# Performance work log

Hardware: AMD Instinct MI355X
Metric: run time of the kernel (lower is better)

## Reference

```python
import math
import jax, jax.numpy as jnp
import numpy as np


def setup_inputs() -> dict:
    key = jax.random.key(0)
    kq, kk, kv = jax.random.split(key, 3)
    bs, n_tok, n_heads, width = 2, 2048, 8, 64
    deg = 32  # neighbors per dst token -> coo_cnt_max
    q = jax.random.normal(kq, (bs, n_tok, n_heads, width), dtype=jnp.float32)
    k = jax.random.normal(kk, (bs, n_tok, n_heads, width), dtype=jnp.float32)
    v = jax.random.normal(kv, (bs, n_tok, n_heads, width), dtype=jnp.float32)
    rng = np.random.default_rng(0)
    dst = np.repeat(np.arange(n_tok), deg)            # [cl]
    src = rng.integers(0, n_tok, size=n_tok * deg)    # [cl]
    sm = np.tile(np.arange(deg), n_tok)               # [cl], unique per dst
    coo = jnp.asarray(np.stack([dst, src, sm], axis=1), dtype=jnp.int32)  # [cl,3]
    return {"q": q, "k": k, "v": v, "coo": coo, "coo_cnt_max": deg}


def reference(q, k, v, coo, coo_cnt_max):
    bs, n_tok, n_heads, width = q.shape
    dst, src, sm = coo[:, 0], coo[:, 1], coo[:, 2]
    # [b, h, t, w] layout
    qq = q.transpose(0, 2, 1, 3)
    kk = k.transpose(0, 2, 1, 3)
    vv = v.transpose(0, 2, 1, 3)
    scale = -1.0 / math.sqrt(width)
    # per-edge negative scaled L1 distance: [b, h, cl]
    ww = jnp.sum(jnp.abs(qq[:, :, dst, :] - kk[:, :, src, :]), axis=-1) * scale
    neg_big = jnp.asarray(-1e32, dtype=q.dtype)
    # scatter edge scores into dense padded attention slots: [b, h, t, cnt+1]
    attn = jnp.full((bs, n_heads, n_tok, coo_cnt_max + 1), neg_big, dtype=q.dtype)
    attn = attn.at[:, :, dst, sm].set(ww)
    attn_sm = jax.nn.softmax(attn, axis=-1)
    # scatter values into padded neighbor-value tensor: [b, h, t, cnt+1, w]
    vw = jnp.zeros((bs, n_heads, n_tok, coo_cnt_max + 1, width), dtype=q.dtype)
    vw = vw.at[:, :, dst, sm, :].set(vv[:, :, src, :])
    vo = jnp.einsum('bhds,bhdsw->bdhw', attn_sm, vw)
    # only dst tokens appearing in coo receive output; others stay zero
    vout = jnp.zeros_like(v).at[:, dst, :, :].set(vo[:, dst, :, :])
    return vout
```

## Files before the change

kernel.cpp:

```cpp
#include <hip/hip_runtime.h>

#define BS   2
#define NT   2048
#define NH   8
#define WD   64
#define DEG  32

__global__ __launch_bounds__(64) void l1attn_sparse_kernel(
    const float* __restrict__ q,
    const float* __restrict__ k,
    const float* __restrict__ v,
    const int* __restrict__ coo,
    float* __restrict__ out)
{
    const int bid   = blockIdx.x;
    const int combo = bid & 7;
    const int hp    = combo & 3;
    const int b     = combo >> 2;
    const int t     = bid >> 3;
    const int ln    = threadIdx.x;
    const int hw    = ln >> 5;
    const int l     = ln & 31;

    __shared__ int   s_src[DEG];
    __shared__ float s_q[2 * WD];
    __shared__ float s_k[DEG * 2 * WD];

    if (ln < DEG) {
        s_src[ln] = coo[(t * DEG + ln) * 3 + 1];
    }
    {
        const float2* qrow = (const float2*)
            (q + ((size_t)(b * NT + t) * NH + hp * 2) * WD);
        float2 qv = qrow[ln];
        s_q[2 * ln]     = qv.x;
        s_q[2 * ln + 1] = qv.y;
    }
    __syncthreads();

    {
        const int c = l;
        #pragma unroll
        for (int r = 0; r < 16; ++r) {
            const int j = 2 * r + hw;
            const int s = s_src[j];
            const int chunk = (c + j) & 31;
            const float* gaddr = k + ((size_t)(b * NT + s) * NH + hp * 2) * WD
                               + chunk * 4;
            float* laddr = s_k + 2 * r * (2 * WD);
            __builtin_amdgcn_global_load_lds(
                (const __attribute__((address_space(1))) void*)gaddr,
                (__attribute__((address_space(3))) void*)laddr,
                16, 0, 0);
        }
    }

    const int h  = hp * 2 + hw;
    const int jg = l >> 4;
    const int wq = l & 15;
    float4 vr[16];
    #pragma unroll
    for (int i = 0; i < 16; ++i) {
        const int sv = s_src[2 * i + jg];
        vr[i] = *(const float4*)(v + ((size_t)(b * NT + sv) * NH + h) * WD + 4 * wq);
    }

    __syncthreads();

    const float* qh = s_q + hw * WD;
    float acc = 0.f;
    #pragma unroll
    for (int i = 0; i < 16; ++i) {
        const int slot = ((hw * 16 + i) - l) & 31;
        float4 kv = *(const float4*)(s_k + l * (2 * WD) + slot * 4);
        const int wb = i * 4;
        acc += fabsf(qh[wb]     - kv.x);
        acc += fabsf(qh[wb + 1] - kv.y);
        acc += fabsf(qh[wb + 2] - kv.z);
        acc += fabsf(qh[wb + 3] - kv.w);
    }
    float logit = -0.125f * acc;

    float m = logit;
    #pragma unroll
    for (int d = 16; d >= 1; d >>= 1) m = fmaxf(m, __shfl_xor(m, d));
    float e = __expf(logit - m);
    float ssum = e;
    #pragma unroll
    for (int d = 16; d >= 1; d >>= 1) ssum += __shfl_xor(ssum, d);
    const float p = e / ssum;

    float4 o4 = make_float4(0.f, 0.f, 0.f, 0.f);
    #pragma unroll
    for (int i = 0; i < 16; ++i) {
        const float pj = __shfl(p, 2 * i + jg, 32);
        o4.x += pj * vr[i].x;
        o4.y += pj * vr[i].y;
        o4.z += pj * vr[i].z;
        o4.w += pj * vr[i].w;
    }
    o4.x += __shfl_xor(o4.x, 16);
    o4.y += __shfl_xor(o4.y, 16);
    o4.z += __shfl_xor(o4.z, 16);
    o4.w += __shfl_xor(o4.w, 16);

    if (jg == 0) {
        *(float4*)(out + ((size_t)(b * NT + t) * NH + h) * WD + 4 * wq) = o4;
    }
}

extern "C" void kernel_launch(void* const* d_in, const int* in_sizes, int n_in,
                              void* d_out, int out_size, void* d_ws, size_t ws_size,
                              hipStream_t stream) {
    const float* q   = (const float*)d_in[0];
    const float* k   = (const float*)d_in[1];
    const float* v   = (const float*)d_in[2];
    const int*   coo = (const int*)d_in[3];
    float*       o   = (float*)d_out;

    dim3 grid(BS * NT * 4);
    dim3 block(64);
    hipLaunchKernelGGL(l1attn_sparse_kernel, grid, block, 0, stream, q, k, v, coo, o);
}
```

Baseline: 106.3 us.

## Pre-pack K and V to bf16 interleaved rows and gather both via LDS

Adds a pre-pass kernel that converts K and V to bf16 and packs them into one 512-byte row per (batch, head-pair, token) in workspace. The main kernel then gathers a single packed row per neighbor into LDS, covering both K and V, and reads V from LDS instead of doing separate per-thread global loads. This halves gather traffic for the random neighbor accesses. It costs an extra kernel launch plus a full pass over K and V, and bf16 rounding reduces accuracy. The fp32 path is kept as a fallback when the workspace is too small.

```diff
diff --git a/kernel.cpp b/kernel.cpp
--- a/kernel.cpp
+++ b/kernel.cpp
@@ -1,4 +1,5 @@
 #include <hip/hip_runtime.h>
+#include <hip/hip_bf16.h>
 
 #define BS   2
 #define NT   2048
@@ -6,7 +7,136 @@
 #define WD   64
 #define DEG  32
 
-__global__ __launch_bounds__(64) void l1attn_sparse_kernel(
+#define PK_ROWS   (BS * 4 * NT)
+#define PK_ROW_B  512
+#define PK_UINTS  (PK_ROWS * (PK_ROW_B / 4))
+
+__device__ __forceinline__ float bfbits_lo(unsigned int u) {
+    unsigned int x = u << 16; float f; __builtin_memcpy(&f, &x, 4); return f;
+}
+__device__ __forceinline__ float bfbits_hi(unsigned int u) {
+    unsigned int x = u & 0xffff0000u; float f; __builtin_memcpy(&f, &x, 4); return f;
+}
+__device__ __forceinline__ unsigned short f2bf(float f) {
+    __hip_bfloat16 h = __float2bfloat16(f);
+    unsigned short u; __builtin_memcpy(&u, &h, 2); return u;
+}
+
+__global__ __launch_bounds__(256) void pack_kv_bf16(
+    const float* __restrict__ k,
+    const float* __restrict__ v,
+    unsigned int* __restrict__ packed)
+{
+    const int u    = blockIdx.x * 256 + threadIdx.x;
+    const int row  = u >> 7;
+    const int pos  = u & 127;
+    const int part = pos >> 6;
+    const int e    = pos & 63;
+    const int s    = row & (NT - 1);
+    const int hp   = (row >> 11) & 3;
+    const int b    = row >> 13;
+    const int elem = e * 2;
+    const int h_in = elem >> 6;
+    const int w0   = elem & 63;
+
+    const float* src = (part == 0 ? k : v)
+        + (((size_t)(b * NT + s) * NH + hp * 2 + h_in) << 6) + w0;
+    float2 f = *(const float2*)src;
+    packed[u] = (unsigned int)f2bf(f.x) | ((unsigned int)f2bf(f.y) << 16);
+}
+
+__global__ __launch_bounds__(64) void l1attn_main_bf16(
+    const float* __restrict__ q,
+    const unsigned int* __restrict__ packed,
+    const int* __restrict__ coo,
+    float* __restrict__ out)
+{
+    const int bid   = blockIdx.x;
+    const int combo = bid & 7;
+    const int hp    = combo & 3;
+    const int b     = combo >> 2;
+    const int t     = bid >> 3;
+    const int ln    = threadIdx.x;
+    const int hw    = ln >> 5;
+    const int l     = ln & 31;
+
+    __shared__ int          s_src[DEG];
+    __shared__ float        s_q[2 * WD];
+    __shared__ unsigned int s_k[DEG * 128];
+
+    if (ln < DEG) {
+        s_src[ln] = coo[(t * DEG + ln) * 3 + 1];
+    }
+    {
+        const float2* qrow = (const float2*)
+            (q + ((size_t)(b * NT + t) * NH + hp * 2) * WD);
+        float2 qv = qrow[ln];
+        s_q[2 * ln]     = qv.x;
+        s_q[2 * ln + 1] = qv.y;
+    }
+    __syncthreads();
+
+    {
+        #pragma unroll
+        for (int r = 0; r < 16; ++r) {
+            const int j = 2 * r + hw;
+            const int s = s_src[j];
+            const int chunk = (l + j) & 31;
+            const char* gaddr = (const char*)packed
+                + ((size_t)((b * 4 + hp) * NT + s)) * PK_ROW_B + chunk * 16;
+            char* laddr = (char*)s_k + 2 * r * PK_ROW_B;
+            __builtin_amdgcn_global_load_lds(
+                (const __attribute__((address_space(1))) void*)gaddr,
+                (__attribute__((address_space(3))) void*)laddr,
+                16, 0, 0);
+        }
+    }
+    __syncthreads();
+
+    const float* qh = s_q + hw * WD;
+    float acc = 0.f;
+    #pragma unroll
+    for (int i = 0; i < 8; ++i) {
+        const int slot = ((hw * 8 + i) - l) & 31;
+        uint4 c = *(const uint4*)((const char*)s_k + l * PK_ROW_B + slot * 16);
+        const int wb = i * 8;
+        const unsigned int ws[4] = {c.x, c.y, c.z, c.w};
+        #pragma unroll
+        for (int m = 0; m < 4; ++m) {
+            acc += fabsf(qh[wb + 2 * m]     - bfbits_lo(ws[m]));
+            acc += fabsf(qh[wb + 2 * m + 1] - bfbits_hi(ws[m]));
+        }
+    }
+    float logit = -0.125f * acc;
+
+    float m = logit;
+    #pragma unroll
+    for (int d = 16; d >= 1; d >>= 1) m = fmaxf(m, __shfl_xor(m, d));
+    float e = __expf(logit - m);
+    float ssum = e;
+    #pragma unroll
+    for (int d = 16; d >= 1; d >>= 1) ssum += __shfl_xor(ssum, d);
+    const float p = e / ssum;
+
+    const int gv   = 16 + hw * 8 + (l >> 2);
+    const int boff = (l & 3) * 4;
+    float o0 = 0.f, o1 = 0.f;
+    #pragma unroll 8
+    for (int j = 0; j < DEG; ++j) {
+        const float pj = __shfl(p, j, 32);
+        const int slot = (gv - j) & 31;
+        unsigned int w = *(const unsigned int*)
+            ((const char*)s_k + j * PK_ROW_B + slot * 16 + boff);
+        o0 += pj * bfbits_lo(w);
+        o1 += pj * bfbits_hi(w);
+    }
+
+    const int h = hp * 2 + hw;
+    float2 res = make_float2(o0, o1);
+    *(float2*)(out + ((size_t)(b * NT + t) * NH + h) * WD + 2 * l) = res;
+}
+
+__global__ __launch_bounds__(64) void l1attn_sparse_fp32(
     const float* __restrict__ q,
     const float* __restrict__ k,
     const float* __restrict__ v,
@@ -26,18 +156,14 @@
     __shared__ float s_q[2 * WD];
     __shared__ float s_k[DEG * 2 * WD];
 
-    if (ln < DEG) {
-        s_src[ln] = coo[(t * DEG + ln) * 3 + 1];
-    }
+    if (ln < DEG) s_src[ln] = coo[(t * DEG + ln) * 3 + 1];
     {
         const float2* qrow = (const float2*)
             (q + ((size_t)(b * NT + t) * NH + hp * 2) * WD);
         float2 qv = qrow[ln];
-        s_q[2 * ln]     = qv.x;
-        s_q[2 * ln + 1] = qv.y;
-    }
-    __syncthreads();
-
+        s_q[2 * ln] = qv.x; s_q[2 * ln + 1] = qv.y;
+    }
+    __syncthreads();
     {
         const int c = l;
         #pragma unroll
@@ -50,11 +176,9 @@
             float* laddr = s_k + 2 * r * (2 * WD);
             __builtin_amdgcn_global_load_lds(
                 (const __attribute__((address_space(1))) void*)gaddr,
-                (__attribute__((address_space(3))) void*)laddr,
-                16, 0, 0);
+                (__attribute__((address_space(3))) void*)laddr, 16, 0, 0);
         }
     }
-
     const int h  = hp * 2 + hw;
     const int jg = l >> 4;
     const int wq = l & 15;
@@ -64,9 +188,7 @@
         const int sv = s_src[2 * i + jg];
         vr[i] = *(const float4*)(v + ((size_t)(b * NT + sv) * NH + h) * WD + 4 * wq);
     }
-
-    __syncthreads();
-
+    __syncthreads();
     const float* qh = s_q + hw * WD;
     float acc = 0.f;
     #pragma unroll
@@ -74,13 +196,10 @@
         const int slot = ((hw * 16 + i) - l) & 31;
         float4 kv = *(const float4*)(s_k + l * (2 * WD) + slot * 4);
         const int wb = i * 4;
-        acc += fabsf(qh[wb]     - kv.x);
-        acc += fabsf(qh[wb + 1] - kv.y);
-        acc += fabsf(qh[wb + 2] - kv.z);
-        acc += fabsf(qh[wb + 3] - kv.w);
+        acc += fabsf(qh[wb] - kv.x) + fabsf(qh[wb + 1] - kv.y)
+             + fabsf(qh[wb + 2] - kv.z) + fabsf(qh[wb + 3] - kv.w);
     }
     float logit = -0.125f * acc;
-
     float m = logit;
     #pragma unroll
     for (int d = 16; d >= 1; d >>= 1) m = fmaxf(m, __shfl_xor(m, d));
@@ -89,24 +208,17 @@
     #pragma unroll
     for (int d = 16; d >= 1; d >>= 1) ssum += __shfl_xor(ssum, d);
     const float p = e / ssum;
-
     float4 o4 = make_float4(0.f, 0.f, 0.f, 0.f);
     #pragma unroll
     for (int i = 0; i < 16; ++i) {
         const float pj = __shfl(p, 2 * i + jg, 32);
-        o4.x += pj * vr[i].x;
-        o4.y += pj * vr[i].y;
-        o4.z += pj * vr[i].z;
-        o4.w += pj * vr[i].w;
-    }
-    o4.x += __shfl_xor(o4.x, 16);
-    o4.y += __shfl_xor(o4.y, 16);
-    o4.z += __shfl_xor(o4.z, 16);
-    o4.w += __shfl_xor(o4.w, 16);
-
-    if (jg == 0) {
+        o4.x += pj * vr[i].x; o4.y += pj * vr[i].y;
+        o4.z += pj * vr[i].z; o4.w += pj * vr[i].w;
+    }
+    o4.x += __shfl_xor(o4.x, 16); o4.y += __shfl_xor(o4.y, 16);
+    o4.z += __shfl_xor(o4.z, 16); o4.w += __shfl_xor(o4.w, 16);
+    if (jg == 0)
         *(float4*)(out + ((size_t)(b * NT + t) * NH + h) * WD + 4 * wq) = o4;
-    }
 }
 
 extern "C" void kernel_launch(void* const* d_in, const int* in_sizes, int n_in,
@@ -118,7 +230,14 @@
     const int*   coo = (const int*)d_in[3];
     float*       o   = (float*)d_out;
 
-    dim3 grid(BS * NT * 4);
-    dim3 block(64);
-    hipLaunchKernelGGL(l1attn_sparse_kernel, grid, block, 0, stream, q, k, v, coo, o);
-}
+    if (ws_size >= (size_t)PK_UINTS * 4) {
+        unsigned int* packed = (unsigned int*)d_ws;
+        hipLaunchKernelGGL(pack_kv_bf16, dim3(PK_UINTS / 256), dim3(256), 0,
+                           stream, k, v, packed);
+        hipLaunchKernelGGL(l1attn_main_bf16, dim3(BS * NT * 4), dim3(64), 0,
+                           stream, q, packed, coo, o);
+    } else {
+        hipLaunchKernelGGL(l1attn_sparse_fp32, dim3(BS * NT * 4), dim3(64), 0,
+                           stream, q, k, v, coo, o);
+    }
+}
```

Measured after the change: 111.3 us. 4.7% more time.
